# Kernel tuning notes

Hardware: AMD Instinct MI355X
Metric: run time of the kernel (lower is better)

The kernel has to match this reference:

```python
import jax, jax.numpy as jnp
import numpy as np

N = 100000       # nodes
E = 3200000      # edges (avg degree 32)
IN = 64          # in_channels
HID = 32         # hidden_channels
HEADS = 2
OUT = 1
EPS = 1e-5       # LayerNorm eps
SLOPE = 0.2      # LeakyReLU negative slope (PyG default)


def setup_inputs() -> dict:
    key = jax.random.key(0)
    ks = jax.random.split(key, 18)
    def nrm(k, shape, scale=0.1):
        return jax.random.normal(k, shape, dtype=jnp.float32) * scale
    return {
        "x": jax.random.normal(ks[0], (N, IN), dtype=jnp.float32),
        "edge_index": jax.random.randint(ks[1], (2, E), 0, N, dtype=jnp.int64),
        # GATConv layer 1 (concat=True)
        "W1": nrm(ks[2], (IN, HEADS * HID)),
        "a_src1": nrm(ks[3], (HEADS, HID)),
        "a_dst1": nrm(ks[4], (HEADS, HID)),
        "b1": jnp.zeros((HEADS * HID,), jnp.float32),
        "ln1_g": jnp.ones((HEADS * HID,), jnp.float32),
        "ln1_b": jnp.zeros((HEADS * HID,), jnp.float32),
        # GATConv layer 2 (heads=1, concat=False)
        "W2": nrm(ks[5], (HEADS * HID, HID)),
        "a_src2": nrm(ks[6], (1, HID)),
        "a_dst2": nrm(ks[7], (1, HID)),
        "b2": jnp.zeros((HID,), jnp.float32),
        "ln2_g": jnp.ones((HID,), jnp.float32),
        "ln2_b": jnp.zeros((HID,), jnp.float32),
        # output Linear
        "Wout": nrm(ks[8], (HID, OUT)),
        "bout": jnp.zeros((OUT,), jnp.float32),
    }


def layer_norm(x, g, b):
    mu = jnp.mean(x, axis=-1, keepdims=True)
    var = jnp.mean(jnp.square(x - mu), axis=-1, keepdims=True)
    return (x - mu) * jax.lax.rsqrt(var + EPS) * g + b


def gat_conv(x, edge_index, W, a_src, a_dst, bias, heads, ch, concat):
    """PyG GATConv (add_self_loops=True, bias=True), eval mode (no dropout)."""
    n = x.shape[0]
    loop = jnp.arange(n, dtype=edge_index.dtype)
    src = jnp.concatenate([edge_index[0], loop])   # [E+N]
    dst = jnp.concatenate([edge_index[1], loop])   # [E+N]
    h = (x @ W).reshape(n, heads, ch)              # [N,H,C]
    al_src = jnp.sum(h * a_src, axis=-1)           # [N,H]
    al_dst = jnp.sum(h * a_dst, axis=-1)           # [N,H]
    logits = jax.nn.leaky_relu(al_src[src] + al_dst[dst], SLOPE)  # [E+N,H]
    # segment softmax over destination nodes
    m = jax.lax.stop_gradient(jax.ops.segment_max(logits, dst, num_segments=n))
    e = jnp.exp(logits - m[dst])
    denom = jax.ops.segment_sum(e, dst, num_segments=n)
    alpha = e / denom[dst]                         # [E+N,H]
    out = jax.ops.segment_sum(h[src] * alpha[:, :, None], dst, num_segments=n)  # [N,H,C]
    out = out.reshape(n, heads * ch) if concat else out.mean(axis=1)
    return out + bias


def reference(x, edge_index, W1, a_src1, a_dst1, b1, ln1_g, ln1_b,
              W2, a_src2, a_dst2, b2, ln2_g, ln2_b, Wout, bout):
    h = gat_conv(x, edge_index, W1, a_src1, a_dst1, b1, HEADS, HID, True)
    h = jax.nn.elu(layer_norm(h, ln1_g, ln1_b))
    h = gat_conv(h, edge_index, W2, a_src2, a_dst2, b2, 1, HID, False)
    h = jax.nn.elu(layer_norm(h, ln2_g, ln2_b))
    return h @ Wout + bout  # [N, OUT]
```

## Files before the change

kernel.cpp:

```cpp
#include <hip/hip_runtime.h>

#define EPS 1e-5f
#define SLOPE 0.2f
#define MAXK 512
#define SEGCAP 12288
#define PBATCH 8192
#define AG1_SLOTS 8
#define AG2_SLOTS 8

__device__ __forceinline__ float leaky(float z) {
    return fmaxf(z, 0.f) + SLOPE * fminf(z, 0.f);
}
__device__ __forceinline__ ushort f2bf(float f) {
    unsigned u = __float_as_uint(f);
    u += 0x7FFFu + ((u >> 16) & 1u);
    return (ushort)(u >> 16);
}
__device__ __forceinline__ float bf2f(ushort b) {
    return __uint_as_float(((unsigned)b) << 16);
}
__device__ __forceinline__ float blo(unsigned u) {
    return __uint_as_float(u << 16);
}
__device__ __forceinline__ float bhi(unsigned u) {
    return __uint_as_float(u & 0xffff0000u);
}
__device__ __forceinline__ void gather16_to_lds(const void* g, void* l) {
    __builtin_amdgcn_global_load_lds(
        (const __attribute__((address_space(1))) void*)g,
        (__attribute__((address_space(3))) void*)l, 16, 0, 0);
}

__global__ __launch_bounds__(1024) void fused1(
    const int* __restrict__ ei, int E, int K, int* __restrict__ segcnt,
    unsigned* __restrict__ part,
    const float* __restrict__ x, const float* __restrict__ W1,
    const float* __restrict__ as1, const float* __restrict__ ad1,
    ushort* __restrict__ h1b, float* __restrict__ al_s, float* __restrict__ al_d,
    int N, int EB) {
    __shared__ float smem[4096 + 64 * 68];
    int t = threadIdx.x;
    if ((int)blockIdx.x < EB) {
        int* h   = (int*)smem;
        int* gp  = h + 512;
        int* run = h + 1024;
        for (int i = t; i < K; i += 1024) { h[i] = 0; run[i] = 0; }
        __syncthreads();
        int base = blockIdx.x * PBATCH;
        int sv[PBATCH / 1024], dv[PBATCH / 1024];
#pragma unroll
        for (int j = 0; j < PBATCH / 1024; j++) {
            int e = base + j * 1024 + t;
            sv[j] = (e < E) ? ei[e] : -1;
            dv[j] = (e < E) ? ei[E + e] : -1;
            if (dv[j] >= 0) atomicAdd(&h[dv[j] >> 8], 1);
        }
        __syncthreads();
        for (int i = t; i < K; i += 1024)
            gp[i] = h[i] ? atomicAdd(&segcnt[i * 16], h[i]) : 0;
        __syncthreads();
#pragma unroll
        for (int j = 0; j < PBATCH / 1024; j++) {
            if (dv[j] >= 0) {
                int b = dv[j] >> 8;
                int p = atomicAdd(&run[b], 1) + gp[b];
                if (p < SEGCAP)
                    part[(size_t)b * SEGCAP + p] =
                        ((unsigned)sv[j] << 8) | (unsigned)(dv[j] & 255);
            }
        }
        return;
    }
    float* Ws = smem;
    float (*xs)[68] = (float(*)[68])(smem + 4096);
    for (int i = t; i < 4096; i += 1024) Ws[i] = W1[i];
    int base = (blockIdx.x - EB) * 64;
    {
        int rr = t >> 4, kk = t & 15;
        int gr = base + rr;
        float4 vx = (gr < N) ? ((const float4*)x)[(size_t)gr * 16 + kk]
                             : make_float4(0.f, 0.f, 0.f, 0.f);
        *(float4*)&xs[rr][kk * 4] = vx;
    }
    __syncthreads();
    int wv = t >> 6, c = t & 63;
    int r0 = base + wv * 4;
    float acc0 = 0.f, acc1 = 0.f, acc2 = 0.f, acc3 = 0.f;
#pragma unroll
    for (int k = 0; k < 64; k += 4) {
        float4 x0 = *(const float4*)&xs[wv * 4 + 0][k];
        float4 x1 = *(const float4*)&xs[wv * 4 + 1][k];
        float4 x2 = *(const float4*)&xs[wv * 4 + 2][k];
        float4 x3 = *(const float4*)&xs[wv * 4 + 3][k];
        float w0 = Ws[(k + 0) * 64 + c];
        float w1 = Ws[(k + 1) * 64 + c];
        float w2 = Ws[(k + 2) * 64 + c];
        float w3 = Ws[(k + 3) * 64 + c];
        acc0 = fmaf(x0.x, w0, acc0); acc1 = fmaf(x1.x, w0, acc1);
        acc2 = fmaf(x2.x, w0, acc2); acc3 = fmaf(x3.x, w0, acc3);
        acc0 = fmaf(x0.y, w1, acc0); acc1 = fmaf(x1.y, w1, acc1);
        acc2 = fmaf(x2.y, w1, acc2); acc3 = fmaf(x3.y, w1, acc3);
        acc0 = fmaf(x0.z, w2, acc0); acc1 = fmaf(x1.z, w2, acc1);
        acc2 = fmaf(x2.z, w2, acc2); acc3 = fmaf(x3.z, w2, acc3);
        acc0 = fmaf(x0.w, w3, acc0); acc1 = fmaf(x1.w, w3, acc1);
        acc2 = fmaf(x2.w, w3, acc2); acc3 = fmaf(x3.w, w3, acc3);
    }
    int head = c >> 5, cc = c & 31;
    float asc = as1[head * 32 + cc], adc = ad1[head * 32 + cc];
    float vs0 = acc0 * asc, vd0 = acc0 * adc;
    float vs1 = acc1 * asc, vd1 = acc1 * adc;
    float vs2 = acc2 * asc, vd2 = acc2 * adc;
    float vs3 = acc3 * asc, vd3 = acc3 * adc;
#pragma unroll
    for (int off = 1; off < 32; off <<= 1) {
        vs0 += __shfl_xor(vs0, off); vd0 += __shfl_xor(vd0, off);
        vs1 += __shfl_xor(vs1, off); vd1 += __shfl_xor(vd1, off);
        vs2 += __shfl_xor(vs2, off); vd2 += __shfl_xor(vd2, off);
        vs3 += __shfl_xor(vs3, off); vd3 += __shfl_xor(vd3, off);
    }
    if (r0 + 0 < N) h1b[(size_t)(r0 + 0) * 64 + c] = f2bf(acc0);
    if (r0 + 1 < N) h1b[(size_t)(r0 + 1) * 64 + c] = f2bf(acc1);
    if (r0 + 2 < N) h1b[(size_t)(r0 + 2) * 64 + c] = f2bf(acc2);
    if (r0 + 3 < N) h1b[(size_t)(r0 + 3) * 64 + c] = f2bf(acc3);
    if (cc == 0) {
        if (r0 + 0 < N) { al_s[(r0 + 0) * 2 + head] = vs0; al_d[(r0 + 0) * 2 + head] = vd0; }
        if (r0 + 1 < N) { al_s[(r0 + 1) * 2 + head] = vs1; al_d[(r0 + 1) * 2 + head] = vd1; }
        if (r0 + 2 < N) { al_s[(r0 + 2) * 2 + head] = vs2; al_d[(r0 + 2) * 2 + head] = vd2; }
        if (r0 + 3 < N) { al_s[(r0 + 3) * 2 + head] = vs3; al_d[(r0 + 3) * 2 + head] = vd3; }
    }
}

__global__ __launch_bounds__(1024) void sortseg(
    const int* __restrict__ segcnt, int N,
    unsigned* __restrict__ part, int* __restrict__ nodeofs, int* __restrict__ cnt,
    int* __restrict__ perm) {
    __shared__ int h2[4096];
    __shared__ int ex[256];
    __shared__ int wsum[4];
    __shared__ unsigned outb[SEGCAP];
    int b = blockIdx.x, t = threadIdx.x;
    int lane = t & 63;
    size_t base = (size_t)b * SEGCAP;
    int sz = min(segcnt[b * 16], SEGCAP);
    for (int i = t; i < 4096; i += 1024) h2[i] = 0;
    __syncthreads();
    for (int i = t; i < sz; i += 1024) {
        unsigned code = part[base + i];
        int key = ((code & 255) << 4) | ((code >> 21) & 15);
        atomicAdd(&h2[key], 1);
    }
    __syncthreads();
    int v = 0;
    if (t < 256) {
#pragma unroll
        for (int i = 0; i < 16; i++) v += h2[t * 16 + i];
    }
    int incl = v;
#pragma unroll
    for (int off = 1; off < 64; off <<= 1) {
        int y = __shfl_up(incl, off);
        if (lane >= off) incl += y;
    }
    if (t < 256 && lane == 63) wsum[t >> 6] = incl;
    __syncthreads();
    if (t < 256) {
        int w = t >> 6;
        int wpre = 0;
#pragma unroll
        for (int k = 0; k < 4; k++) if (k < w) wpre += wsum[k];
        int exv = incl + wpre - v;
        int run = exv;
#pragma unroll
        for (int i = 0; i < 16; i++) {
            int lc = h2[t * 16 + i];
            h2[t * 16 + i] = run;
            run += lc;
        }
        int n = b * 256 + t;
        if (n < N) { cnt[n] = v; nodeofs[n] = (int)(base + exv); }
    }
    __syncthreads();
    for (int i = t; i < sz; i += 1024) {
        unsigned code = part[base + i];
        int key = ((code & 255) << 4) | ((code >> 21) & 15);
        int p = atomicAdd(&h2[key], 1);
        outb[p] = code >> 8;
    }
    __syncthreads();
    for (int i = t; i < sz; i += 1024) part[base + i] = outb[i];
    __syncthreads();
    if (t < 256) h2[t] = 0;
    __syncthreads();
    int n = b * 256 + t;
    int dbin = min(v, 255);
    if (t < 256 && n < N) atomicAdd(&h2[dbin], 1);
    __syncthreads();
    int hv = (t < 256) ? h2[t] : 0;
    int incl2 = hv;
#pragma unroll
    for (int off = 1; off < 64; off <<= 1) {
        int y = __shfl_up(incl2, off);
        if (lane >= off) incl2 += y;
    }
    if (t < 256 && lane == 63) wsum[t >> 6] = incl2;
    __syncthreads();
    if (t < 256) {
        int w = t >> 6;
        int wpre = 0;
#pragma unroll
        for (int k = 0; k < 4; k++) if (k < w) wpre += wsum[k];
        ex[t] = incl2 + wpre - hv;
    }
    __syncthreads();
    if (t < 256 && n < N) {
        int r = atomicAdd(&ex[dbin], 1);
        perm[b * 256 + r] = n;
    }
}

__global__ __launch_bounds__(256) void aggB1(
    const ushort* __restrict__ h1b, const float* __restrict__ als,
    const float* __restrict__ ald, const int* __restrict__ nodeofs,
    const int* __restrict__ cnt, const unsigned* __restrict__ csr,
    const int* __restrict__ perm,
    const float* __restrict__ b1, const float* __restrict__ g1,
    const float* __restrict__ bb1,
    const float* __restrict__ W2, const float* __restrict__ as2,
    const float* __restrict__ ad2, ushort* __restrict__ h2b,
    float* __restrict__ al2s, float* __restrict__ al2d, int N) {
    __shared__ uint4 stage[4][AG1_SLOTS * 64];
    __shared__ float W2s[64 * 32];
    int t = threadIdx.x;
    for (int i = t; i < 2048; i += 256) W2s[i] = W2[i];
    __syncthreads();
    int wid = t >> 6, lane = t & 63;
    int grp = lane >> 3, q = lane & 7;
    int gbase = grp << 3;
    uint4* mystage = stage[wid];
    int idx = blockIdx.x * 32 + wid * 8 + grp;
    bool valid = idx < N;
    int nc = perm[min(idx, N - 1)];
    int head = q >> 2;
    const float2* als2 = (const float2*)als;
    const float2* ald2 = (const float2*)ald;
    float2 adv = ald2[nc], asv = als2[nc];
    float ad0 = adv.x, ad1v = adv.y;
    float wsf = __expf(leaky((head ? asv.y : asv.x) + (head ? ad1v : ad0)));
    const uint4* h4 = (const uint4*)h1b;
    uint4 hs = h4[(size_t)nc * 8 + q];
    float a0 = wsf * blo(hs.x), a1 = wsf * bhi(hs.x);
    float a2 = wsf * blo(hs.y), a3 = wsf * bhi(hs.y);
    float a4 = wsf * blo(hs.z), a5 = wsf * bhi(hs.z);
    float a6 = wsf * blo(hs.w), a7 = wsf * bhi(hs.w);
    float lp0 = 0.f, lp1 = 0.f;
    int ofs = valid ? nodeofs[nc] : 0;
    int deg = valid ? cnt[nc] : 0;
    int degm1 = max(deg - 1, 0);
    int degmax = deg;
    degmax = max(degmax, __shfl_xor(degmax, 8));
    degmax = max(degmax, __shfl_xor(degmax, 16));
    degmax = max(degmax, __shfl_xor(degmax, 32));
    int sq = 0;
    if (degmax > 0) sq = min((int)csr[ofs + min(q, degm1)], N - 1);
    for (int eb = 0; eb < degmax; eb += AG1_SLOTS) {
#pragma unroll
        for (int k = 0; k < AG1_SLOTS; k++) {
            int s = __shfl(sq, gbase + k);
            gather16_to_lds(h4 + ((size_t)s * 8 + q), &mystage[k * 64]);
        }
        float2 av = als2[sq];
        int nsq = sq;
        int ebn = eb + AG1_SLOTS;
        if (ebn < degmax)
            nsq = min((int)csr[ofs + min(ebn + q, degm1)], N - 1);
        bool ev = (eb + q < deg);
        float w0 = ev ? __expf(leaky(av.x + ad0)) : 0.f;
        float w1 = ev ? __expf(leaky(av.y + ad1v)) : 0.f;
        lp0 += w0;
        lp1 += w1;
        asm volatile("s_waitcnt vmcnt(0)" ::: "memory");
        __builtin_amdgcn_sched_barrier(0);
#pragma unroll
        for (int k = 0; k < AG1_SLOTS; k++) {
            float wk0 = __shfl(w0, gbase + k);
            float wk1 = __shfl(w1, gbase + k);
            float w = head ? wk1 : wk0;
            uint4 hv = mystage[k * 64 + lane];
            a0 = fmaf(w, blo(hv.x), a0); a1 = fmaf(w, bhi(hv.x), a1);
            a2 = fmaf(w, blo(hv.y), a2); a3 = fmaf(w, bhi(hv.y), a3);
            a4 = fmaf(w, blo(hv.z), a4); a5 = fmaf(w, bhi(hv.z), a5);
            a6 = fmaf(w, blo(hv.w), a6); a7 = fmaf(w, bhi(hv.w), a7);
        }
        sq = nsq;
    }
#pragma unroll
    for (int off = 1; off < 8; off <<= 1) {
        lp0 += __shfl_xor(lp0, off);
        lp1 += __shfl_xor(lp1, off);
    }
    if (!valid) return;
    float l = (head ? lp1 : lp0) + wsf;
    float inv = 1.f / l;
    float4 bA = ((const float4*)b1)[2 * q];
    float4 bB = ((const float4*)b1)[2 * q + 1];
    float v0 = a0 * inv + bA.x, v1 = a1 * inv + bA.y;
    float v2 = a2 * inv + bA.z, v3 = a3 * inv + bA.w;
    float v4 = a4 * inv + bB.x, v5 = a5 * inv + bB.y;
    float v6 = a6 * inv + bB.z, v7 = a7 * inv + bB.w;
    float s1 = v0 + v1 + v2 + v3 + v4 + v5 + v6 + v7;
#pragma unroll
    for (int off = 1; off < 8; off <<= 1) s1 += __shfl_xor(s1, off);
    float mu = s1 * (1.f / 64.f);
    float d0 = v0 - mu, d1 = v1 - mu, d2 = v2 - mu, d3 = v3 - mu;
    float d4 = v4 - mu, d5 = v5 - mu, d6 = v6 - mu, d7 = v7 - mu;
    float s2v = d0 * d0 + d1 * d1 + d2 * d2 + d3 * d3
              + d4 * d4 + d5 * d5 + d6 * d6 + d7 * d7;
#pragma unroll
    for (int off = 1; off < 8; off <<= 1) s2v += __shfl_xor(s2v, off);
    float rs = rsqrtf(s2v * (1.f / 64.f) + EPS);
    float4 gA = ((const float4*)g1)[2 * q];
    float4 gB = ((const float4*)g1)[2 * q + 1];
    float4 cA = ((const float4*)bb1)[2 * q];
    float4 cB = ((const float4*)bb1)[2 * q + 1];
    float ya[8];
    ya[0] = d0 * rs * gA.x + cA.x;
    ya[1] = d1 * rs * gA.y + cA.y;
    ya[2] = d2 * rs * gA.z + cA.z;
    ya[3] = d3 * rs * gA.w + cA.w;
    ya[4] = d4 * rs * gB.x + cB.x;
    ya[5] = d5 * rs * gB.y + cB.y;
    ya[6] = d6 * rs * gB.z + cB.z;
    ya[7] = d7 * rs * gB.w + cB.w;
#pragma unroll
    for (int j = 0; j < 8; j++)
        ya[j] = (ya[j] > 0.f) ? ya[j] : (__expf(ya[j]) - 1.f);
    float o0 = 0.f, o1 = 0.f, o2 = 0.f, o3 = 0.f;
#pragma unroll
    for (int src = 0; src < 8; src++) {
#pragma unroll
        for (int j = 0; j < 8; j++) {
            float yv = __shfl(ya[j], gbase + src);
            float4 wr = *(const float4*)&W2s[(src * 8 + j) * 32 + 4 * q];
            o0 = fmaf(yv, wr.x, o0);
            o1 = fmaf(yv, wr.y, o1);
            o2 = fmaf(yv, wr.z, o2);
            o3 = fmaf(yv, wr.w, o3);
        }
    }
    ((ushort4*)h2b)[(size_t)nc * 8 + q] =
        make_ushort4(f2bf(o0), f2bf(o1), f2bf(o2), f2bf(o3));
    float4 a2v = ((const float4*)as2)[q];
    float4 d2v = ((const float4*)ad2)[q];
    float ps = o0 * a2v.x + o1 * a2v.y + o2 * a2v.z + o3 * a2v.w;
    float pd = o0 * d2v.x + o1 * d2v.y + o2 * d2v.z + o3 * d2v.w;
    ps += __shfl_xor(ps, 1); ps += __shfl_xor(ps, 2); ps += __shfl_xor(ps, 4);
    pd += __shfl_xor(pd, 1); pd += __shfl_xor(pd, 2); pd += __shfl_xor(pd, 4);
    if (q == 0) { al2s[nc] = ps; al2d[nc] = pd; }
}

__global__ __launch_bounds__(256) void aggB2(
    const ushort* __restrict__ h2b, const float* __restrict__ als,
    const float* __restrict__ ald, const int* __restrict__ nodeofs,
    const int* __restrict__ cnt, const unsigned* __restrict__ csr,
    const int* __restrict__ perm,
    const float* __restrict__ b2, const float* __restrict__ g2,
    const float* __restrict__ bb2, const float* __restrict__ Wout,
    const float* __restrict__ bout, float* __restrict__ out, int N) {
    __shared__ uint4 stage[4][AG2_SLOTS * 64];
    int t = threadIdx.x;
    int wid = t >> 6, lane = t & 63;
    int grp = lane >> 2, q = lane & 3;
    int gbase = grp << 2;
    uint4* mystage = stage[wid];
    int idx = blockIdx.x * 64 + wid * 16 + grp;
    bool valid = idx < N;
    int nc = perm[min(idx, N - 1)];
    float myad = ald[nc];
    float wsf = __expf(leaky(als[nc] + myad));
    const uint4* h4 = (const uint4*)h2b;
    uint4 hs = h4[(size_t)nc * 4 + q];
    float a0 = wsf * blo(hs.x), a1 = wsf * bhi(hs.x);
    float a2 = wsf * blo(hs.y), a3 = wsf * bhi(hs.y);
    float a4 = wsf * blo(hs.z), a5 = wsf * bhi(hs.z);
    float a6 = wsf * blo(hs.w), a7 = wsf * bhi(hs.w);
    float lp = 0.f;
    int ofs = valid ? nodeofs[nc] : 0;
    int deg = valid ? cnt[nc] : 0;
    int degm1 = max(deg - 1, 0);
    int degmax = deg;
    degmax = max(degmax, __shfl_xor(degmax, 4));
    degmax = max(degmax, __shfl_xor(degmax, 8));
    degmax = max(degmax, __shfl_xor(degmax, 16));
    degmax = max(degmax, __shfl_xor(degmax, 32));
    int sq0 = 0, sq1 = 0;
    if (degmax > 0) {
        sq0 = min((int)csr[ofs + min(q, degm1)], N - 1);
        sq1 = min((int)csr[ofs + min(4 + q, degm1)], N - 1);
    }
    for (int eb = 0; eb < degmax; eb += AG2_SLOTS) {
#pragma unroll
        for (int k = 0; k < AG2_SLOTS; k++) {
            int s = (k < 4) ? __shfl(sq0, gbase + k)
                            : __shfl(sq1, gbase + (k - 4));
            gather16_to_lds(h4 + ((size_t)s * 4 + q), &mystage[k * 64]);
        }
        float av0 = als[sq0];
        float av1 = als[sq1];
        int nsq0 = sq0, nsq1 = sq1;
        int ebn = eb + AG2_SLOTS;
        if (ebn < degmax) {
            nsq0 = min((int)csr[ofs + min(ebn + q, degm1)], N - 1);
            nsq1 = min((int)csr[ofs + min(ebn + 4 + q, degm1)], N - 1);
        }
        float wq0 = (eb + q < deg) ? __expf(leaky(av0 + myad)) : 0.f;
        float wq1 = (eb + 4 + q < deg) ? __expf(leaky(av1 + myad)) : 0.f;
        lp += wq0 + wq1;
        asm volatile("s_waitcnt vmcnt(0)" ::: "memory");
        __builtin_amdgcn_sched_barrier(0);
#pragma unroll
        for (int k = 0; k < AG2_SLOTS; k++) {
            float w = (k < 4) ? __shfl(wq0, gbase + k)
                              : __shfl(wq1, gbase + (k - 4));
            uint4 hv = mystage[k * 64 + lane];
            a0 = fmaf(w, blo(hv.x), a0); a1 = fmaf(w, bhi(hv.x), a1);
            a2 = fmaf(w, blo(hv.y), a2); a3 = fmaf(w, bhi(hv.y), a3);
            a4 = fmaf(w, blo(hv.z), a4); a5 = fmaf(w, bhi(hv.z), a5);
            a6 = fmaf(w, blo(hv.w), a6); a7 = fmaf(w, bhi(hv.w), a7);
        }
        sq0 = nsq0;
        sq1 = nsq1;
    }
    lp += __shfl_xor(lp, 1);
    lp += __shfl_xor(lp, 2);
    if (!valid) return;
    float l = lp + wsf;
    float inv = 1.f / l;
    float4 bA = ((const float4*)b2)[2 * q];
    float4 bB = ((const float4*)b2)[2 * q + 1];
    float v0 = a0 * inv + bA.x, v1 = a1 * inv + bA.y;
    float v2 = a2 * inv + bA.z, v3 = a3 * inv + bA.w;
    float v4 = a4 * inv + bB.x, v5 = a5 * inv + bB.y;
    float v6 = a6 * inv + bB.z, v7 = a7 * inv + bB.w;
    float s1 = v0 + v1 + v2 + v3 + v4 + v5 + v6 + v7;
    s1 += __shfl_xor(s1, 1); s1 += __shfl_xor(s1, 2);
    float mu = s1 * (1.f / 32.f);
    float d0 = v0 - mu, d1 = v1 - mu, d2 = v2 - mu, d3 = v3 - mu;
    float d4 = v4 - mu, d5 = v5 - mu, d6 = v6 - mu, d7 = v7 - mu;
    float s2v = d0 * d0 + d1 * d1 + d2 * d2 + d3 * d3
              + d4 * d4 + d5 * d5 + d6 * d6 + d7 * d7;
    s2v += __shfl_xor(s2v, 1); s2v += __shfl_xor(s2v, 2);
    float rs = rsqrtf(s2v * (1.f / 32.f) + EPS);
    float4 gA = ((const float4*)g2)[2 * q];
    float4 gB = ((const float4*)g2)[2 * q + 1];
    float4 cA = ((const float4*)bb2)[2 * q];
    float4 cB = ((const float4*)bb2)[2 * q + 1];
    float y0 = d0 * rs * gA.x + cA.x;
    float y1 = d1 * rs * gA.y + cA.y;
    float y2 = d2 * rs * gA.z + cA.z;
    float y3 = d3 * rs * gA.w + cA.w;
    float y4 = d4 * rs * gB.x + cB.x;
    float y5 = d5 * rs * gB.y + cB.y;
    float y6 = d6 * rs * gB.z + cB.z;
    float y7 = d7 * rs * gB.w + cB.w;
    y0 = (y0 > 0.f) ? y0 : (__expf(y0) - 1.f);
    y1 = (y1 > 0.f) ? y1 : (__expf(y1) - 1.f);
    y2 = (y2 > 0.f) ? y2 : (__expf(y2) - 1.f);
    y3 = (y3 > 0.f) ? y3 : (__expf(y3) - 1.f);
    y4 = (y4 > 0.f) ? y4 : (__expf(y4) - 1.f);
    y5 = (y5 > 0.f) ? y5 : (__expf(y5) - 1.f);
    y6 = (y6 > 0.f) ? y6 : (__expf(y6) - 1.f);
    y7 = (y7 > 0.f) ? y7 : (__expf(y7) - 1.f);
    float4 wA = ((const float4*)Wout)[2 * q];
    float4 wB = ((const float4*)Wout)[2 * q + 1];
    float p = y0 * wA.x + y1 * wA.y + y2 * wA.z + y3 * wA.w
            + y4 * wB.x + y5 * wB.y + y6 * wB.z + y7 * wB.w;
    p += __shfl_xor(p, 1); p += __shfl_xor(p, 2);
    if (q == 0) out[nc] = p + bout[0];
}

extern "C" void kernel_launch(void* const* d_in, const int* in_sizes, int n_in,
                              void* d_out, int out_size, void* d_ws, size_t ws_size,
                              hipStream_t stream) {
    const float* x    = (const float*)d_in[0];
    const int*   ei   = (const int*)d_in[1];
    const float* W1   = (const float*)d_in[2];
    const float* as1  = (const float*)d_in[3];
    const float* ad1  = (const float*)d_in[4];
    const float* b1   = (const float*)d_in[5];
    const float* g1   = (const float*)d_in[6];
    const float* bb1  = (const float*)d_in[7];
    const float* W2   = (const float*)d_in[8];
    const float* as2  = (const float*)d_in[9];
    const float* ad2  = (const float*)d_in[10];
    const float* b2   = (const float*)d_in[11];
    const float* g2   = (const float*)d_in[12];
    const float* bb2  = (const float*)d_in[13];
    const float* Wout = (const float*)d_in[14];
    const float* bout = (const float*)d_in[15];
    float* out = (float*)d_out;

    const int N = in_sizes[0] / 64;
    const int E = in_sizes[1] / 2;
    const int K = (N + 255) / 256;

    auto align_up = [](size_t v) { return (v + 255) & ~(size_t)255; };
    char* ws = (char*)d_ws;
    unsigned* part    = (unsigned*)ws; ws += align_up((size_t)K * SEGCAP * 4);
    int*      segcnt  = (int*)ws;      ws += align_up((size_t)MAXK * 16 * 4);
    int*      nodeofs = (int*)ws;      ws += align_up((size_t)N * 4);
    int*      cnt     = (int*)ws;      ws += align_up((size_t)N * 4);
    int*      perm    = (int*)ws;      ws += align_up((size_t)(K * 256) * 4);
    ushort*   h1b     = (ushort*)ws;   ws += align_up((size_t)N * 64 * 2);
    ushort*   h2b     = (ushort*)ws;   ws += align_up((size_t)N * 32 * 2);
    float*    al1s    = (float*)ws;    ws += align_up((size_t)N * 2 * 4);
    float*    al1d    = (float*)ws;    ws += align_up((size_t)N * 2 * 4);
    float*    al2s    = (float*)ws;    ws += align_up((size_t)N * 4);
    float*    al2d    = (float*)ws;    ws += align_up((size_t)N * 4);

    const int EB = (E + PBATCH - 1) / PBATCH;
    const int PB = (N + 63) / 64;

    hipMemsetAsync(segcnt, 0, (size_t)K * 16 * 4, stream);
    fused1<<<EB + PB, 1024, 0, stream>>>(ei, E, K, segcnt, part,
                                         x, W1, as1, ad1, h1b, al1s, al1d, N, EB);
    sortseg<<<K, 1024, 0, stream>>>(segcnt, N, part, nodeofs, cnt, perm);
    aggB1<<<(N + 31) / 32, 256, 0, stream>>>(h1b, al1s, al1d, nodeofs, cnt, part,
                                             perm, b1, g1, bb1,
                                             W2, as2, ad2, h2b, al2s, al2d, N);
    aggB2<<<(N + 63) / 64, 256, 0, stream>>>(h2b, al2s, al2d, nodeofs, cnt, part,
                                             perm, b2, g2, bb2, Wout, bout, out, N);
}
```

Measured before the change: 300.7 us.

## Merge both aggregation kernels into one persistent cooperative kernel with grid sync

Turns the two GAT aggregation kernels into device functions and runs them from a single persistent cooperative kernel of 1024 blocks that loops over tiles, with a grid-wide barrier between the layers. The aim is to remove one kernel launch and the drain/ramp gap between layer 1 and layer 2, and to load W2 into shared memory once per block rather than once per tile. In exchange it needs a grid barrier, and the persistent loop may balance load worse than one block per tile. If the cooperative launch fails, it falls back to the original two launches.

Result: slower. 470.3 us (+56.4%).

```diff
diff --git a/kernel.cpp b/kernel.cpp
--- a/kernel.cpp
+++ b/kernel.cpp
@@ -1,4 +1,7 @@
 #include <hip/hip_runtime.h>
+#include <hip/hip_cooperative_groups.h>
+
+namespace cg = cooperative_groups;
 
 #define EPS 1e-5f
 #define SLOPE 0.2f
@@ -218,26 +221,22 @@
     }
 }
 
-__global__ __launch_bounds__(256) void aggB1(
+__device__ __forceinline__ void agg1_body(
+    int tile, uint4* stageAll, const float* W2s,
     const ushort* __restrict__ h1b, const float* __restrict__ als,
     const float* __restrict__ ald, const int* __restrict__ nodeofs,
     const int* __restrict__ cnt, const unsigned* __restrict__ csr,
-    const int* __restrict__ perm,
-    const float* __restrict__ b1, const float* __restrict__ g1,
-    const float* __restrict__ bb1,
-    const float* __restrict__ W2, const float* __restrict__ as2,
-    const float* __restrict__ ad2, ushort* __restrict__ h2b,
-    float* __restrict__ al2s, float* __restrict__ al2d, int N) {
-    __shared__ uint4 stage[4][AG1_SLOTS * 64];
-    __shared__ float W2s[64 * 32];
+    const int* __restrict__ perm, const float* __restrict__ b1,
+    const float* __restrict__ g1, const float* __restrict__ bb1,
+    const float* __restrict__ as2, const float* __restrict__ ad2,
+    ushort* __restrict__ h2b, float* __restrict__ al2s,
+    float* __restrict__ al2d, int N) {
     int t = threadIdx.x;
-    for (int i = t; i < 2048; i += 256) W2s[i] = W2[i];
-    __syncthreads();
     int wid = t >> 6, lane = t & 63;
     int grp = lane >> 3, q = lane & 7;
     int gbase = grp << 3;
-    uint4* mystage = stage[wid];
-    int idx = blockIdx.x * 32 + wid * 8 + grp;
+    uint4* mystage = stageAll + wid * (AG1_SLOTS * 64);
+    int idx = tile * 32 + wid * 8 + grp;
     bool valid = idx < N;
     int nc = perm[min(idx, N - 1)];
     int head = q >> 2;
@@ -358,7 +357,8 @@
     if (q == 0) { al2s[nc] = ps; al2d[nc] = pd; }
 }
 
-__global__ __launch_bounds__(256) void aggB2(
+__device__ __forceinline__ void agg2_body(
+    int tile, uint4* stageAll,
     const ushort* __restrict__ h2b, const float* __restrict__ als,
     const float* __restrict__ ald, const int* __restrict__ nodeofs,
     const int* __restrict__ cnt, const unsigned* __restrict__ csr,
@@ -366,13 +366,12 @@
     const float* __restrict__ b2, const float* __restrict__ g2,
     const float* __restrict__ bb2, const float* __restrict__ Wout,
     const float* __restrict__ bout, float* __restrict__ out, int N) {
-    __shared__ uint4 stage[4][AG2_SLOTS * 64];
     int t = threadIdx.x;
     int wid = t >> 6, lane = t & 63;
     int grp = lane >> 2, q = lane & 3;
     int gbase = grp << 2;
-    uint4* mystage = stage[wid];
-    int idx = blockIdx.x * 64 + wid * 16 + grp;
+    uint4* mystage = stageAll + wid * (AG2_SLOTS * 64);
+    int idx = tile * 64 + wid * 16 + grp;
     bool valid = idx < N;
     int nc = perm[min(idx, N - 1)];
     float myad = ald[nc];
@@ -478,6 +477,67 @@
     if (q == 0) out[nc] = p + bout[0];
 }
 
+__global__ __launch_bounds__(256) void aggB1(
+    const ushort* __restrict__ h1b, const float* __restrict__ als,
+    const float* __restrict__ ald, const int* __restrict__ nodeofs,
+    const int* __restrict__ cnt, const unsigned* __restrict__ csr,
+    const int* __restrict__ perm,
+    const float* __restrict__ b1, const float* __restrict__ g1,
+    const float* __restrict__ bb1,
+    const float* __restrict__ W2, const float* __restrict__ as2,
+    const float* __restrict__ ad2, ushort* __restrict__ h2b,
+    float* __restrict__ al2s, float* __restrict__ al2d, int N) {
+    __shared__ uint4 stage[4 * AG1_SLOTS * 64];
+    __shared__ float W2s[64 * 32];
+    int t = threadIdx.x;
+    for (int i = t; i < 2048; i += 256) W2s[i] = W2[i];
+    __syncthreads();
+    agg1_body(blockIdx.x, stage, W2s, h1b, als, ald, nodeofs, cnt, csr, perm,
+              b1, g1, bb1, as2, ad2, h2b, al2s, al2d, N);
+}
+
+__global__ __launch_bounds__(256) void aggB2(
+    const ushort* __restrict__ h2b, const float* __restrict__ als,
+    const float* __restrict__ ald, const int* __restrict__ nodeofs,
+    const int* __restrict__ cnt, const unsigned* __restrict__ csr,
+    const int* __restrict__ perm,
+    const float* __restrict__ b2, const float* __restrict__ g2,
+    const float* __restrict__ bb2, const float* __restrict__ Wout,
+    const float* __restrict__ bout, float* __restrict__ out, int N) {
+    __shared__ uint4 stage[4 * AG2_SLOTS * 64];
+    agg2_body(blockIdx.x, stage, h2b, als, ald, nodeofs, cnt, csr, perm,
+              b2, g2, bb2, Wout, bout, out, N);
+}
+
+__global__ __launch_bounds__(256, 4) void tail2(
+    const ushort* __restrict__ h1b, const float* __restrict__ als1,
+    const float* __restrict__ ald1, const int* __restrict__ nodeofs,
+    const int* __restrict__ cnt, const unsigned* __restrict__ csr,
+    const int* __restrict__ perm, const float* __restrict__ b1,
+    const float* __restrict__ g1, const float* __restrict__ bb1,
+    const float* __restrict__ W2, const float* __restrict__ as2,
+    const float* __restrict__ ad2, ushort* __restrict__ h2b,
+    float* __restrict__ al2s, float* __restrict__ al2d,
+    const float* __restrict__ b2, const float* __restrict__ g2,
+    const float* __restrict__ bb2, const float* __restrict__ Wout,
+    const float* __restrict__ bout, float* __restrict__ out, int N) {
+    __shared__ uint4 stage[4 * AG1_SLOTS * 64];
+    __shared__ float W2s[64 * 32];
+    cg::grid_group grid = cg::this_grid();
+    int t = threadIdx.x;
+    for (int i = t; i < 2048; i += 256) W2s[i] = W2[i];
+    __syncthreads();
+    const int nT1 = (N + 31) / 32;
+    for (int tile = blockIdx.x; tile < nT1; tile += gridDim.x)
+        agg1_body(tile, stage, W2s, h1b, als1, ald1, nodeofs, cnt, csr, perm,
+                  b1, g1, bb1, as2, ad2, h2b, al2s, al2d, N);
+    grid.sync();
+    const int nT2 = (N + 63) / 64;
+    for (int tile = blockIdx.x; tile < nT2; tile += gridDim.x)
+        agg2_body(tile, stage, h2b, al2s, al2d, nodeofs, cnt, csr, perm,
+                  b2, g2, bb2, Wout, bout, out, N);
+}
+
 extern "C" void kernel_launch(void* const* d_in, const int* in_sizes, int n_in,
                               void* d_out, int out_size, void* d_ws, size_t ws_size,
                               hipStream_t stream) {
@@ -499,7 +559,7 @@
     const float* bout = (const float*)d_in[15];
     float* out = (float*)d_out;
 
-    const int N = in_sizes[0] / 64;
+    int N = in_sizes[0] / 64;
     const int E = in_sizes[1] / 2;
     const int K = (N + 255) / 256;
 
@@ -524,9 +584,33 @@
     fused1<<<EB + PB, 1024, 0, stream>>>(ei, E, K, segcnt, part,
                                          x, W1, as1, ad1, h1b, al1s, al1d, N, EB);
     sortseg<<<K, 1024, 0, stream>>>(segcnt, N, part, nodeofs, cnt, perm);
-    aggB1<<<(N + 31) / 32, 256, 0, stream>>>(h1b, al1s, al1d, nodeofs, cnt, part,
-                                             perm, b1, g1, bb1,
-                                             W2, as2, ad2, h2b, al2s, al2d, N);
-    aggB2<<<(N + 63) / 64, 256, 0, stream>>>(h2b, al2s, al2d, nodeofs, cnt, part,
-                                             perm, b2, g2, bb2, Wout, bout, out, N);
-}
+
+    const ushort* h1b_c = h1b;
+    const float* al1s_c = al1s;
+    const float* al1d_c = al1d;
+    const int* nodeofs_c = nodeofs;
+    const int* cnt_c = cnt;
+    const unsigned* csr_c = part;
+    const int* perm_c = perm;
+    ushort* h2b_c = h2b;
+    float* al2s_c = al2s;
+    float* al2d_c = al2d;
+    void* args[] = {
+        (void*)&h1b_c, (void*)&al1s_c, (void*)&al1d_c, (void*)&nodeofs_c,
+        (void*)&cnt_c, (void*)&csr_c, (void*)&perm_c, (void*)&b1,
+        (void*)&g1, (void*)&bb1, (void*)&W2, (void*)&as2, (void*)&ad2,
+        (void*)&h2b_c, (void*)&al2s_c, (void*)&al2d_c,
+        (void*)&b2, (void*)&g2, (void*)&bb2, (void*)&Wout,
+        (void*)&bout, (void*)&out, (void*)&N
+    };
+    hipError_t err = hipLaunchCooperativeKernel(
+        (const void*)tail2, dim3(1024), dim3(256), args, 0, stream);
+    if (err != hipSuccess) {
+        aggB1<<<(N + 31) / 32, 256, 0, stream>>>(
+            h1b, al1s, al1d, nodeofs, cnt, part, perm, b1, g1, bb1,
+            W2, as2, ad2, h2b, al2s, al2d, N);
+        aggB2<<<(N + 63) / 64, 256, 0, stream>>>(
+            h2b, al2s, al2d, nodeofs, cnt, part, perm,
+            b2, g2, bb2, Wout, bout, out, N);
+    }
+}
```
